# Performance work log

Hardware: AMD Instinct MI355X
Metric: run time of the kernel (lower is better)

Reference implementation:

```python
import jax, jax.numpy as jnp
import numpy as np

DIM, SEQ, HEADS = 1024, 2048, 8
HEAD_DIM = DIM // HEADS


def setup_inputs() -> dict:
    key = jax.random.key(0)
    ks = jax.random.split(key, 8)
    x = jax.random.normal(ks[0], (4, SEQ, DIM), dtype=jnp.float32)
    # Linear weights stored [in, out]; y = x @ W + b (same math as torch Linear).
    Wk = jax.random.normal(ks[1], (DIM, DIM), dtype=jnp.float32) * (DIM ** -0.5)
    bk = jnp.zeros((DIM,), dtype=jnp.float32)
    Wv = jax.random.normal(ks[2], (DIM, DIM), dtype=jnp.float32) * (DIM ** -0.5)
    bv = jnp.zeros((DIM,), dtype=jnp.float32)
    # learned AFT position bias [heads, seq, seq]; small scale keeps exp stable
    w_aft = jax.random.normal(ks[3], (HEADS, SEQ, SEQ), dtype=jnp.float32) * 0.1
    Wo = jax.random.normal(ks[4], (DIM, DIM), dtype=jnp.float32) * (DIM ** -0.5)
    bo = jnp.zeros((DIM,), dtype=jnp.float32)
    return {"x": x, "Wk": Wk, "bk": bk, "Wv": Wv, "bv": bv,
            "w_aft": w_aft, "Wo": Wo, "bo": bo}


def reference(x, Wk, bk, Wv, bv, w_aft, Wo, bo):
    N, S, _ = x.shape
    k = (x @ Wk + bk).reshape(N, S, HEADS, HEAD_DIM)
    v = (x @ Wv + bv).reshape(N, S, HEADS, HEAD_DIM)
    ek = jnp.exp(k)  # [N,S,H,D]
    # causal mask: position t attends to i <= t; exp(w+k) = exp(w)*exp(k)
    causal = jnp.tril(jnp.ones((S, S), dtype=bool))
    ew = jnp.where(causal[None, :, :], jnp.exp(w_aft), 0.0)  # [H,T,S]
    num = jnp.einsum('hts,nshd->nthd', ew, ek * v)  # [N,T,H,D]
    den = jnp.einsum('hts,nshd->nthd', ew, ek)      # [N,T,H,D]
    aft = (num / den).reshape(N, S, DIM)
    return aft @ Wo + bo
```

## Files before the change

kernel.cpp:

```cpp
#include <hip/hip_runtime.h>
#include <hip/hip_bf16.h>
#include <stdint.h>

#define DIM 1024
#define SEQ 2048
#define NB 4
#define HEADS 8
#define HD 128
#define ROWS (NB*SEQ)

typedef __attribute__((ext_vector_type(8))) short bf16x8;
typedef __attribute__((ext_vector_type(4))) float f32x4;

#define VMCNT(n) asm volatile("s_waitcnt vmcnt(" #n ")" ::: "memory")
#define SBAR()   __builtin_amdgcn_s_barrier()
#define SCHED0() __builtin_amdgcn_sched_barrier(0)

static __device__ __forceinline__ unsigned short f2bf(float f){
  union { float f; unsigned int u; } x; x.f = f;
  unsigned int r = x.u + 0x7fffu + ((x.u >> 16) & 1u);
  return (unsigned short)(r >> 16);
}

static __device__ __forceinline__ void gld_lds16(const void* g, void* l){
  __builtin_amdgcn_global_load_lds(
      (const __attribute__((address_space(1))) void*)g,
      (__attribute__((address_space(3))) void*)l,
      16, 0, 0);
}

__global__ void k_prep(const float* __restrict__ x,
                       const float* __restrict__ Wk, const float* __restrict__ Wv,
                       const float* __restrict__ Wo, const float* __restrict__ waft,
                       unsigned short* __restrict__ xb,
                       unsigned short* __restrict__ Tk, unsigned short* __restrict__ Tv,
                       unsigned short* __restrict__ To, unsigned short* __restrict__ ewb){
  __shared__ float tile[64][65];
  const int B = blockIdx.x;
  const int tid = threadIdx.x;
  if (B < 2048){
    for (int i = B*256 + tid; i < ROWS*DIM/4; i += 2048*256){
      const float4 v = reinterpret_cast<const float4*>(x)[i];
      ushort4 o;
      o.x = f2bf(v.x); o.y = f2bf(v.y); o.z = f2bf(v.z); o.w = f2bf(v.w);
      reinterpret_cast<ushort4*>(xb)[i] = o;
    }
  } else if (B < 2816){
    const int D = B - 2048;
    const int z = D >> 8;
    const int rem = D & 255;
    const int bo = (rem & 15) * 64;
    const int bi = (rem >> 4) * 64;
    const float* W = (z == 0) ? Wk : (z == 1) ? Wv : Wo;
    unsigned short* WT = (z == 0) ? Tk : (z == 1) ? Tv : To;
    #pragma unroll
    for (int it = 0; it < 16; ++it){
      int f = it*256 + tid;
      int r = f >> 6, c = f & 63;
      tile[r][c] = W[(size_t)(bi + r) * DIM + bo + c];
    }
    __syncthreads();
    #pragma unroll
    for (int it = 0; it < 16; ++it){
      int f = it*256 + tid;
      int r = f >> 6, c = f & 63;
      WT[(size_t)(bo + r) * DIM + bi + c] = f2bf(tile[c][r]);
    }
  } else {
    const int row = (B - 2816) * 4 + (tid >> 6);
    const int lane = tid & 63;
    const int t = row & 2047;
    const int h = row >> 11;
    const float* src = waft + ((size_t)h*SEQ + t) * SEQ;
    unsigned short* dst = ewb + ((size_t)h*SEQ + t) * SEQ;
    const int smax4 = ((t & ~127) + 128) >> 2;
    for (int i = lane; i < smax4; i += 64){
      const float4 w4 = reinterpret_cast<const float4*>(src)[i];
      const int s = i * 4;
      ushort4 o;
      o.x = (s+0 <= t) ? f2bf(__expf(w4.x)) : (unsigned short)0;
      o.y = (s+1 <= t) ? f2bf(__expf(w4.y)) : (unsigned short)0;
      o.z = (s+2 <= t) ? f2bf(__expf(w4.z)) : (unsigned short)0;
      o.w = (s+3 <= t) ? f2bf(__expf(w4.w)) : (unsigned short)0;
      reinterpret_cast<ushort4*>(dst)[i] = o;
    }
  }
}

__global__ __launch_bounds__(512) void k_proj(
    const unsigned short* __restrict__ xb,
    const unsigned short* __restrict__ wkt,
    const unsigned short* __restrict__ wvt,
    const float* __restrict__ bk,
    const float* __restrict__ bv,
    unsigned short* __restrict__ ekb)
{
  __shared__ __align__(16) char smem[131072];
  unsigned short* Asl = (unsigned short*)smem;
  unsigned short* Bsl = (unsigned short*)(smem + 65536);
  float* xch = (float*)smem;

  const int tid  = threadIdx.x;
  const int lane = tid & 63;
  const int lo   = lane & 15;
  const int hi   = lane >> 4;
  const int wid  = tid >> 6;
  const int wm   = wid >> 2;
  const int wn   = wid & 3;
  const int D    = blockIdx.x;
  const int mb   = D >> 3;
  const int cb   = D & 7;
  const int row0 = mb * 256;
  const int col0k = cb * 128;

  f32x4 acc[8][4] = {};

  auto stage_unit = [&](int kt, int slot, int u){
    const int half = u & 1;
    const bool isB = (u >> 1) != 0;
    unsigned short* lb = (isB ? Bsl : Asl) + slot*(256*64) + half*(128*64);
    const unsigned short* gb;
    if (!isB)           gb = xb  + (size_t)(row0 + half*128)*DIM + kt*64;
    else if (half == 0) gb = wkt + (size_t)col0k*DIM + kt*64;
    else                gb = wvt + (size_t)col0k*DIM + kt*64;
    #pragma unroll
    for (int it = 0; it < 2; ++it){
      const int po = (it*512 + tid)*16;
      const int r  = po >> 7;
      const int k2 = (po & 127) ^ ((r & 7) << 4);
      gld_lds16(gb + (size_t)r*DIM + (k2 >> 1), (char*)lb + po);
    }
  };

  #pragma unroll
  for (int u = 0; u < 4; ++u) stage_unit(0, 0, u);

  for (int t = 0; t < 16; ++t){
    const int s = t & 1;
    const bool nxt = (t + 1 < 16);
    const char* Ab = (const char*)(Asl + s*(256*64));
    const char* Bb = (const char*)(Bsl + s*(256*64));
    if (nxt){
      stage_unit(t + 1, s ^ 1, 0);
      stage_unit(t + 1, s ^ 1, 1);
      VMCNT(4);
    } else {
      VMCNT(0);
    }
    SCHED0();
    SBAR();
    SCHED0();
    bf16x8 b[4][2];
    #pragma unroll
    for (int nf = 0; nf < 4; ++nf){
      const int R = wn*64 + nf*16 + lo;
      #pragma unroll
      for (int ks = 0; ks < 2; ++ks){
        const int K2 = (ks*64 + hi*16) ^ ((R & 7) << 4);
        b[nf][ks] = *reinterpret_cast<const bf16x8*>(Bb + R*128 + K2);
      }
    }
    bf16x8 a0[4][2];
    #pragma unroll
    for (int mf = 0; mf < 4; ++mf){
      const int R = wm*128 + mf*16 + lo;
      #pragma unroll
      for (int ks = 0; ks < 2; ++ks){
        const int K2 = (ks*64 + hi*16) ^ ((R & 7) << 4);
        a0[mf][ks] = *reinterpret_cast<const bf16x8*>(Ab + R*128 + K2);
      }
    }
    if (nxt){
      stage_unit(t + 1, s ^ 1, 2);
      stage_unit(t + 1, s ^ 1, 3);
    }
    __builtin_amdgcn_s_setprio(1);
    #pragma unroll
    for (int ks = 0; ks < 2; ++ks)
      #pragma unroll
      for (int mf = 0; mf < 4; ++mf)
        #pragma unroll
        for (int nf = 0; nf < 4; ++nf)
          acc[mf][nf] = __builtin_amdgcn_mfma_f32_16x16x32_bf16(
              a0[mf][ks], b[nf][ks], acc[mf][nf], 0, 0, 0);
    __builtin_amdgcn_s_setprio(0);
    bf16x8 a1[4][2];
    #pragma unroll
    for (int mf = 0; mf < 4; ++mf){
      const int R = wm*128 + (4 + mf)*16 + lo;
      #pragma unroll
      for (int ks = 0; ks < 2; ++ks){
        const int K2 = (ks*64 + hi*16) ^ ((R & 7) << 4);
        a1[mf][ks] = *reinterpret_cast<const bf16x8*>(Ab + R*128 + K2);
      }
    }
    __builtin_amdgcn_s_setprio(1);
    #pragma unroll
    for (int ks = 0; ks < 2; ++ks)
      #pragma unroll
      for (int mf = 0; mf < 4; ++mf)
        #pragma unroll
        for (int nf = 0; nf < 4; ++nf)
          acc[4+mf][nf] = __builtin_amdgcn_mfma_f32_16x16x32_bf16(
              a1[mf][ks], b[nf][ks], acc[4+mf][nf], 0, 0, 0);
    __builtin_amdgcn_s_setprio(0);
    SCHED0();
    SBAR();
  }

  __syncthreads();
  if (wn >= 2){
    #pragma unroll
    for (int mf = 0; mf < 8; ++mf){
      const int rloc = wm*128 + mf*16 + hi*4;
      #pragma unroll
      for (int nf = 0; nf < 4; ++nf){
        const int cv = (wn - 2)*64 + nf*16 + lo;
        #pragma unroll
        for (int jj = 0; jj < 4; ++jj)
          xch[(size_t)(rloc + jj)*128 + cv] = acc[mf][nf][jj];
      }
    }
  }
  __syncthreads();
  if (wn < 2){
    #pragma unroll
    for (int nf = 0; nf < 4; ++nf){
      const int ck = wn*64 + nf*16 + lo;
      const int c  = col0k + ck;
      const int h  = c >> 7;
      const int d  = c & 127;
      const float bkc = bk[c];
      const float bvc = bv[c];
      #pragma unroll
      for (int mf = 0; mf < 8; ++mf){
        const int rloc = wm*128 + mf*16 + hi*4;
        const int r = row0 + rloc;
        const int n = r >> 11;
        const int sidx = r & 2047;
        ushort4 pk, pv;
        #pragma unroll
        for (int jj = 0; jj < 4; ++jj){
          const float kval = acc[mf][nf][jj] + bkc;
          const float vval = xch[(size_t)(rloc + jj)*128 + ck] + bvc;
          const float ek = __expf(kval);
          ((unsigned short*)&pk)[jj] = f2bf(ek);
          ((unsigned short*)&pv)[jj] = f2bf(ek * vval);
        }
        const size_t idx = ((size_t)h*1024 + n*256 + d) * SEQ + sidx;
        *reinterpret_cast<ushort4*>(&ekb[idx]) = pk;
        *reinterpret_cast<ushort4*>(&ekb[idx + (size_t)128*SEQ]) = pv;
      }
    }
  }
}

__global__ __launch_bounds__(512) void k_core(
    const unsigned short* __restrict__ ewb,
    const unsigned short* __restrict__ ekb,
    unsigned short* __restrict__ aftb)
{
  __shared__ __align__(16) char smem[98304];
  unsigned short* Asl = (unsigned short*)smem;
  unsigned short* Bsl = (unsigned short*)(smem + 32768);
  float* xch = (float*)smem;

  const int tid  = threadIdx.x;
  const int lane = tid & 63;
  const int lo   = lane & 15;
  const int hi   = lane >> 4;
  const int wid  = tid >> 6;
  const int wm   = wid >> 2;
  const int wn   = wid & 3;
  const int D  = blockIdx.x;
  const int h  = D & 7;
  const int r_ = D >> 3;
  const int p  = r_ >> 2;
  const int n  = r_ & 3;

  const unsigned short* slab = ekb + ((size_t)h*1024 + n*256) * SEQ;

  #pragma unroll
  for (int half = 0; half < 2; ++half){
    const int tt = half ? p : (15 - p);
    const int t0 = tt * 128;
    const int nst = 2*tt + 2;
    const unsigned short* abase = ewb + ((size_t)h*SEQ + t0) * SEQ;

    f32x4 acc[4][4] = {};

    auto stage_unit = [&](int st, int slot, int u){
      const int s0 = st * 64;
      const int po = tid * 16;
      const int r  = po >> 7;
      const int k2 = (po & 127) ^ ((r & 7) << 4);
      if (u < 2){
        unsigned short* lb = Asl + slot*(128*64) + u*(64*64);
        gld_lds16(abase + (size_t)(u*64 + r)*SEQ + s0 + (k2 >> 1), (char*)lb + po);
      } else {
        unsigned short* lb = Bsl + slot*(256*64) + (u-2)*(64*64);
        gld_lds16(slab + (size_t)((u-2)*64 + r)*SEQ + s0 + (k2 >> 1), (char*)lb + po);
      }
    };

    #pragma unroll
    for (int u = 0; u < 6; ++u) stage_unit(0, 0, u);

    for (int t = 0; t < nst; ++t){
      const int s = t & 1;
      const bool nxt = (t + 1 < nst);
      const char* Ab = (const char*)(Asl + s*(128*64));
      const char* Bb = (const char*)(Bsl + s*(256*64));
      if (nxt){
        stage_unit(t + 1, s ^ 1, 0);
        stage_unit(t + 1, s ^ 1, 1);
        stage_unit(t + 1, s ^ 1, 2);
        VMCNT(3);
      } else {
        VMCNT(0);
      }
      SCHED0();
      SBAR();
      SCHED0();
      bf16x8 b[4][2];
      #pragma unroll
      for (int nf = 0; nf < 4; ++nf){
        const int R = wn*64 + nf*16 + lo;
        #pragma unroll
        for (int ks = 0; ks < 2; ++ks){
          const int K2 = (ks*64 + hi*16) ^ ((R & 7) << 4);
          b[nf][ks] = *reinterpret_cast<const bf16x8*>(Bb + R*128 + K2);
        }
      }
      bf16x8 a0[2][2];
      #pragma unroll
      for (int mf = 0; mf < 2; ++mf){
        const int R = wm*64 + mf*16 + lo;
        #pragma unroll
        for (int ks = 0; ks < 2; ++ks){
          const int K2 = (ks*64 + hi*16) ^ ((R & 7) << 4);
          a0[mf][ks] = *reinterpret_cast<const bf16x8*>(Ab + R*128 + K2);
        }
      }
      if (nxt){
        stage_unit(t + 1, s ^ 1, 3);
        stage_unit(t + 1, s ^ 1, 4);
        stage_unit(t + 1, s ^ 1, 5);
      }
      __builtin_amdgcn_s_setprio(1);
      #pragma unroll
      for (int ks = 0; ks < 2; ++ks)
        #pragma unroll
        for (int mf = 0; mf < 2; ++mf)
          #pragma unroll
          for (int nf = 0; nf < 4; ++nf)
            acc[mf][nf] = __builtin_amdgcn_mfma_f32_16x16x32_bf16(
                a0[mf][ks], b[nf][ks], acc[mf][nf], 0, 0, 0);
      __builtin_amdgcn_s_setprio(0);
      bf16x8 a1[2][2];
      #pragma unroll
      for (int mf = 0; mf < 2; ++mf){
        const int R = wm*64 + (2 + mf)*16 + lo;
        #pragma unroll
        for (int ks = 0; ks < 2; ++ks){
          const int K2 = (ks*64 + hi*16) ^ ((R & 7) << 4);
          a1[mf][ks] = *reinterpret_cast<const bf16x8*>(Ab + R*128 + K2);
        }
      }
      __builtin_amdgcn_s_setprio(1);
      #pragma unroll
      for (int ks = 0; ks < 2; ++ks)
        #pragma unroll
        for (int mf = 0; mf < 2; ++mf)
          #pragma unroll
          for (int nf = 0; nf < 4; ++nf)
            acc[2+mf][nf] = __builtin_amdgcn_mfma_f32_16x16x32_bf16(
                a1[mf][ks], b[nf][ks], acc[2+mf][nf], 0, 0, 0);
      __builtin_amdgcn_s_setprio(0);
      SCHED0();
      SBAR();
    }

    __syncthreads();
    if (wn >= 2){
      #pragma unroll
      for (int mf = 0; mf < 4; ++mf){
        const int rloc = wm*64 + mf*16 + hi*4;
        #pragma unroll
        for (int nf = 0; nf < 4; ++nf){
          const int dv = (wn - 2)*64 + nf*16 + lo;
          #pragma unroll
          for (int jj = 0; jj < 4; ++jj)
            xch[(size_t)(rloc + jj)*129 + dv] = acc[mf][nf][jj];
        }
      }
    }
    __syncthreads();
    if (wn < 2){
      #pragma unroll
      for (int nf = 0; nf < 4; ++nf){
        const int d = wn*64 + nf*16 + lo;
        #pragma unroll
        for (int mf = 0; mf < 4; ++mf){
          const int rloc = wm*64 + mf*16 + hi*4;
          #pragma unroll
          for (int jj = 0; jj < 4; ++jj){
            const int t = t0 + rloc + jj;
            const float num = xch[(size_t)(rloc + jj)*129 + d];
            aftb[((size_t)n*SEQ + t)*DIM + h*HD + d] = f2bf(num / acc[mf][nf][jj]);
          }
        }
      }
    }
    __syncthreads();
  }
}

__global__ __launch_bounds__(512) void k_out(
    const unsigned short* __restrict__ aftb,
    const unsigned short* __restrict__ wot,
    const float* __restrict__ bo,
    float* __restrict__ out)
{
  __shared__ __align__(16) char smem[98304];
  unsigned short* Asl = (unsigned short*)smem;
  unsigned short* Bsl = (unsigned short*)(smem + 32768);

  const int tid  = threadIdx.x;
  const int lane = tid & 63;
  const int lo   = lane & 15;
  const int hi   = lane >> 4;
  const int wid  = tid >> 6;
  const int wm   = wid >> 2;
  const int wn   = wid & 3;
  const int D    = blockIdx.x;
  const int row0 = (D >> 2) * 128;
  const int col0 = (D & 3) * 256;

  f32x4 acc[4][4] = {};

  auto stage_unit = [&](int kt, int slot, int u){
    const int po = tid * 16;
    const int r  = po >> 7;
    const int k2 = (po & 127) ^ ((r & 7) << 4);
    if (u < 2){
      unsigned short* lb = Asl + slot*(128*64) + u*(64*64);
      gld_lds16(aftb + (size_t)(row0 + u*64 + r)*DIM + kt*64 + (k2 >> 1), (char*)lb + po);
    } else {
      unsigned short* lb = Bsl + slot*(256*64) + (u-2)*(64*64);
      gld_lds16(wot + (size_t)(col0 + (u-2)*64 + r)*DIM + kt*64 + (k2 >> 1), (char*)lb + po);
    }
  };

  #pragma unroll
  for (int u = 0; u < 6; ++u) stage_unit(0, 0, u);

  for (int t = 0; t < 16; ++t){
    const int s = t & 1;
    const bool nxt = (t + 1 < 16);
    const char* Ab = (const char*)(Asl + s*(128*64));
    const char* Bb = (const char*)(Bsl + s*(256*64));
    if (nxt){
      stage_unit(t + 1, s ^ 1, 0);
      stage_unit(t + 1, s ^ 1, 1);
      stage_unit(t + 1, s ^ 1, 2);
      VMCNT(3);
    } else {
      VMCNT(0);
    }
    SCHED0();
    SBAR();
    SCHED0();
    bf16x8 b[4][2];
    #pragma unroll
    for (int nf = 0; nf < 4; ++nf){
      const int R = wn*64 + nf*16 + lo;
      #pragma unroll
      for (int ks = 0; ks < 2; ++ks){
        const int K2 = (ks*64 + hi*16) ^ ((R & 7) << 4);
        b[nf][ks] = *reinterpret_cast<const bf16x8*>(Bb + R*128 + K2);
      }
    }
    bf16x8 a0[2][2];
    #pragma unroll
    for (int mf = 0; mf < 2; ++mf){
      const int R = wm*64 + mf*16 + lo;
      #pragma unroll
      for (int ks = 0; ks < 2; ++ks){
        const int K2 = (ks*64 + hi*16) ^ ((R & 7) << 4);
        a0[mf][ks] = *reinterpret_cast<const bf16x8*>(Ab + R*128 + K2);
      }
    }
    if (nxt){
      stage_unit(t + 1, s ^ 1, 3);
      stage_unit(t + 1, s ^ 1, 4);
      stage_unit(t + 1, s ^ 1, 5);
    }
    __builtin_amdgcn_s_setprio(1);
    #pragma unroll
    for (int ks = 0; ks < 2; ++ks)
      #pragma unroll
      for (int mf = 0; mf < 2; ++mf)
        #pragma unroll
        for (int nf = 0; nf < 4; ++nf)
          acc[mf][nf] = __builtin_amdgcn_mfma_f32_16x16x32_bf16(
              a0[mf][ks], b[nf][ks], acc[mf][nf], 0, 0, 0);
    __builtin_amdgcn_s_setprio(0);
    bf16x8 a1[2][2];
    #pragma unroll
    for (int mf = 0; mf < 2; ++mf){
      const int R = wm*64 + (2 + mf)*16 + lo;
      #pragma unroll
      for (int ks = 0; ks < 2; ++ks){
        const int K2 = (ks*64 + hi*16) ^ ((R & 7) << 4);
        a1[mf][ks] = *reinterpret_cast<const bf16x8*>(Ab + R*128 + K2);
      }
    }
    __builtin_amdgcn_s_setprio(1);
    #pragma unroll
    for (int ks = 0; ks < 2; ++ks)
      #pragma unroll
      for (int mf = 0; mf < 2; ++mf)
        #pragma unroll
        for (int nf = 0; nf < 4; ++nf)
          acc[2+mf][nf] = __builtin_amdgcn_mfma_f32_16x16x32_bf16(
              a1[mf][ks], b[nf][ks], acc[2+mf][nf], 0, 0, 0);
    __builtin_amdgcn_s_setprio(0);
    SCHED0();
    SBAR();
  }

  #pragma unroll
  for (int nf = 0; nf < 4; ++nf){
    const int c = col0 + wn*64 + nf*16 + lo;
    const float boc = bo[c];
    #pragma unroll
    for (int mf = 0; mf < 4; ++mf){
      #pragma unroll
      for (int jj = 0; jj < 4; ++jj){
        const int r = row0 + wm*64 + mf*16 + hi*4 + jj;
        out[(size_t)r*DIM + c] = acc[mf][nf][jj] + boc;
      }
    }
  }
}

extern "C" void kernel_launch(void* const* d_in, const int* in_sizes, int n_in,
                              void* d_out, int out_size, void* d_ws, size_t ws_size,
                              hipStream_t stream){
  const float* x    = (const float*)d_in[0];
  const float* Wk   = (const float*)d_in[1];
  const float* bk   = (const float*)d_in[2];
  const float* Wv   = (const float*)d_in[3];
  const float* bv   = (const float*)d_in[4];
  const float* waft = (const float*)d_in[5];
  const float* Wo   = (const float*)d_in[6];
  const float* bo   = (const float*)d_in[7];
  float* out = (float*)d_out;

  char* w = (char*)d_ws;
  unsigned short* xb   = (unsigned short*)w; w += (size_t)ROWS*DIM*2;
  unsigned short* wkt  = (unsigned short*)w; w += (size_t)DIM*DIM*2;
  unsigned short* wvt  = (unsigned short*)w; w += (size_t)DIM*DIM*2;
  unsigned short* wot  = (unsigned short*)w; w += (size_t)DIM*DIM*2;
  unsigned short* ekb  = (unsigned short*)w; w += (size_t)HEADS*1024*SEQ*2;
  unsigned short* aftb = (unsigned short*)w; w += (size_t)ROWS*DIM*2;
  unsigned short* ewb  = (unsigned short*)w; w += (size_t)HEADS*SEQ*SEQ*2;

  k_prep<<<6912, 256, 0, stream>>>(x, Wk, Wv, Wo, waft, xb, wkt, wvt, wot, ewb);
  k_proj<<<256, 512, 0, stream>>>(xb, wkt, wvt, bk, bv, ekb);
  k_core<<<256, 512, 0, stream>>>(ewb, ekb, aftb);
  k_out<<<256, 512, 0, stream>>>(aftb, wot, bo, out);
}
```

Measured before the change: 139.5 us.

## Switch core and output GEMM loops to triple-buffered LDS with one barrier

Both GEMM kernels now rotate three LDS stages instead of two. Each iteration issues all six tile loads for the next stage at once and drops the trailing barrier, so there is one barrier per iteration and loads can overlap compute on the slot just freed. LDS per block grows to 144 KB. The cost is possibly lower occupancy, plus reliance on the three-slot rotation to avoid write-after-read hazards without the second barrier.

Result: no change. 139.1 us, median of 2 (-0.2%).

```diff
diff --git a/kernel.cpp b/kernel.cpp
--- a/kernel.cpp
+++ b/kernel.cpp
@@ -260,9 +260,9 @@
     const unsigned short* __restrict__ ekb,
     unsigned short* __restrict__ aftb)
 {
-  __shared__ __align__(16) char smem[98304];
+  __shared__ __align__(16) char smem[147456];
   unsigned short* Asl = (unsigned short*)smem;
-  unsigned short* Bsl = (unsigned short*)(smem + 32768);
+  unsigned short* Bsl = (unsigned short*)(smem + 49152);
   float* xch = (float*)smem;
 
   const int tid  = threadIdx.x;
@@ -306,16 +306,16 @@
     #pragma unroll
     for (int u = 0; u < 6; ++u) stage_unit(0, 0, u);
 
+    int slot_cur = 0;
     for (int t = 0; t < nst; ++t){
-      const int s = t & 1;
       const bool nxt = (t + 1 < nst);
-      const char* Ab = (const char*)(Asl + s*(128*64));
-      const char* Bb = (const char*)(Bsl + s*(256*64));
+      const int slot_nxt = (slot_cur == 2) ? 0 : slot_cur + 1;
+      const char* Ab = (const char*)(Asl + slot_cur*(128*64));
+      const char* Bb = (const char*)(Bsl + slot_cur*(256*64));
       if (nxt){
-        stage_unit(t + 1, s ^ 1, 0);
-        stage_unit(t + 1, s ^ 1, 1);
-        stage_unit(t + 1, s ^ 1, 2);
-        VMCNT(3);
+        #pragma unroll
+        for (int u = 0; u < 6; ++u) stage_unit(t + 1, slot_nxt, u);
+        VMCNT(6);
       } else {
         VMCNT(0);
       }
@@ -341,11 +341,6 @@
           const int K2 = (ks*64 + hi*16) ^ ((R & 7) << 4);
           a0[mf][ks] = *reinterpret_cast<const bf16x8*>(Ab + R*128 + K2);
         }
-      }
-      if (nxt){
-        stage_unit(t + 1, s ^ 1, 3);
-        stage_unit(t + 1, s ^ 1, 4);
-        stage_unit(t + 1, s ^ 1, 5);
       }
       __builtin_amdgcn_s_setprio(1);
       #pragma unroll
@@ -377,8 +372,7 @@
             acc[2+mf][nf] = __builtin_amdgcn_mfma_f32_16x16x32_bf16(
                 a1[mf][ks], b[nf][ks], acc[2+mf][nf], 0, 0, 0);
       __builtin_amdgcn_s_setprio(0);
-      SCHED0();
-      SBAR();
+      slot_cur = slot_nxt;
     }
 
     __syncthreads();
@@ -422,9 +416,9 @@
     const float* __restrict__ bo,
     float* __restrict__ out)
 {
-  __shared__ __align__(16) char smem[98304];
+  __shared__ __align__(16) char smem[147456];
   unsigned short* Asl = (unsigned short*)smem;
-  unsigned short* Bsl = (unsigned short*)(smem + 32768);
+  unsigned short* Bsl = (unsigned short*)(smem + 49152);
 
   const int tid  = threadIdx.x;
   const int lane = tid & 63;
@@ -455,16 +449,16 @@
   #pragma unroll
   for (int u = 0; u < 6; ++u) stage_unit(0, 0, u);
 
+  int slot_cur = 0;
   for (int t = 0; t < 16; ++t){
-    const int s = t & 1;
     const bool nxt = (t + 1 < 16);
-    const char* Ab = (const char*)(Asl + s*(128*64));
-    const char* Bb = (const char*)(Bsl + s*(256*64));
+    const int slot_nxt = (slot_cur == 2) ? 0 : slot_cur + 1;
+    const char* Ab = (const char*)(Asl + slot_cur*(128*64));
+    const char* Bb = (const char*)(Bsl + slot_cur*(256*64));
     if (nxt){
-      stage_unit(t + 1, s ^ 1, 0);
-      stage_unit(t + 1, s ^ 1, 1);
-      stage_unit(t + 1, s ^ 1, 2);
-      VMCNT(3);
+      #pragma unroll
+      for (int u = 0; u < 6; ++u) stage_unit(t + 1, slot_nxt, u);
+      VMCNT(6);
     } else {
       VMCNT(0);
     }
@@ -490,11 +484,6 @@
         const int K2 = (ks*64 + hi*16) ^ ((R & 7) << 4);
         a0[mf][ks] = *reinterpret_cast<const bf16x8*>(Ab + R*128 + K2);
       }
-    }
-    if (nxt){
-      stage_unit(t + 1, s ^ 1, 3);
-      stage_unit(t + 1, s ^ 1, 4);
-      stage_unit(t + 1, s ^ 1, 5);
     }
     __builtin_amdgcn_s_setprio(1);
     #pragma unroll
@@ -526,8 +515,7 @@
           acc[2+mf][nf] = __builtin_amdgcn_mfma_f32_16x16x32_bf16(
               a1[mf][ks], b[nf][ks], acc[2+mf][nf], 0, 0, 0);
     __builtin_amdgcn_s_setprio(0);
-    SCHED0();
-    SBAR();
+    slot_cur = slot_nxt;
   }
 
   #pragma unroll
```
